# Kernel optimization log

Measured on AMD Instinct MI355X. Metric: run time of the kernel, lower is better.

Reference implementation:

```python
import jax, jax.numpy as jnp
import numpy as np

B, T, VALUE_DIM = 128, 2048, 128
ATTN_DIM, RNN_DIM, NUM_CLASSES = 10, 64, 4000
HS = (RNN_DIM + VALUE_DIM) // 2  # 96
STEPS = 32


def setup_inputs() -> dict:
    key = jax.random.key(0)
    ks = jax.random.split(key, 30)
    def p(k, shape, scale=0.08):
        return jax.random.normal(k, shape, dtype=jnp.float32) * scale
    return {
        "encoder_outputs": jax.random.normal(ks[0], (B, T, VALUE_DIM), dtype=jnp.float32),
        # 2-layer unidirectional GRU (torch layout: W_ih (3H, in), W_hh (3H, H))
        "rnn_w_ih0": p(ks[1], (3 * RNN_DIM, ATTN_DIM)),
        "rnn_w_hh0": p(ks[2], (3 * RNN_DIM, RNN_DIM)),
        "rnn_b_ih0": p(ks[3], (3 * RNN_DIM,)),
        "rnn_b_hh0": p(ks[4], (3 * RNN_DIM,)),
        "rnn_w_ih1": p(ks[5], (3 * RNN_DIM, RNN_DIM)),
        "rnn_w_hh1": p(ks[6], (3 * RNN_DIM, RNN_DIM)),
        "rnn_b_ih1": p(ks[7], (3 * RNN_DIM,)),
        "rnn_b_hh1": p(ks[8], (3 * RNN_DIM,)),
        # location-aware attention
        "attn_conv_w": p(ks[9], (ATTN_DIM, 1, 3)),   # Conv1d(1, A, k=3, pad=1)
        "attn_conv_b": p(ks[10], (ATTN_DIM,)),
        "attn_wq": p(ks[11], (ATTN_DIM, RNN_DIM)),
        "attn_bq": p(ks[12], (ATTN_DIM,)),
        "attn_wv": p(ks[13], (ATTN_DIM, VALUE_DIM)),
        "attn_bias": p(ks[14], (ATTN_DIM,)),
        "attn_score_w": p(ks[15], (ATTN_DIM,)),
        "attn_score_b": p(ks[16], (1,)),
        # classifier MLP: 192 -> 96 -> 48 -> num_classes
        "fc_w1": p(ks[17], (HS, 2 * HS)),
        "fc_b1": p(ks[18], (HS,)),
        "fc_w2": p(ks[19], (HS // 2, HS)),
        "fc_b2": p(ks[20], (HS // 2,)),
        "fc_w3": p(ks[21], (NUM_CLASSES, HS // 2)),
        "fc_b3": p(ks[22], (NUM_CLASSES,)),
        "targets_max_length": STEPS,
    }


def _gru_cell(x, h, w_ih, w_hh, b_ih, b_hh):
    gi = x @ w_ih.T + b_ih
    gh = h @ w_hh.T + b_hh
    i_r, i_z, i_n = jnp.split(gi, 3, axis=-1)
    h_r, h_z, h_n = jnp.split(gh, 3, axis=-1)
    r = jax.nn.sigmoid(i_r + h_r)
    z = jax.nn.sigmoid(i_z + h_z)
    n = jnp.tanh(i_n + r * h_n)
    return (1.0 - z) * n + z * h


def reference(encoder_outputs, rnn_w_ih0, rnn_w_hh0, rnn_b_ih0, rnn_b_hh0,
              rnn_w_ih1, rnn_w_hh1, rnn_b_ih1, rnn_b_hh1,
              attn_conv_w, attn_conv_b, attn_wq, attn_bq, attn_wv, attn_bias,
              attn_score_w, attn_score_b,
              fc_w1, fc_b1, fc_w2, fc_b2, fc_w3, fc_b3, targets_max_length):
    Bn, Tn, _ = encoder_outputs.shape
    H = rnn_w_hh0.shape[1]
    A = rnn_w_ih0.shape[1]
    # value projection is step-invariant: hoist out of the decode loop
    v_proj = jnp.einsum('btv,av->bta', encoder_outputs, attn_wv)  # (B,T,A)
    x0 = jnp.zeros((Bn, A), dtype=encoder_outputs.dtype)  # per-step RNN input

    def step(carry, _):
        h0, h1, last_attn = carry
        h0 = _gru_cell(x0, h0, rnn_w_ih0, rnn_w_hh0, rnn_b_ih0, rnn_b_hh0)
        h1 = _gru_cell(h0, h1, rnn_w_ih1, rnn_w_hh1, rnn_b_ih1, rnn_b_hh1)
        # location feature: Conv1d over previous attention weights
        loc = jax.lax.conv_general_dilated(
            last_attn[:, None, :], attn_conv_w, (1,), 'SAME',
            dimension_numbers=('NCH', 'OIH', 'NCH'))  # (B,A,T)
        loc = jnp.transpose(loc, (0, 2, 1)) + attn_conv_b  # (B,T,A)
        e = jnp.tanh((h1 @ attn_wq.T + attn_bq)[:, None, :] + v_proj + loc + attn_bias)
        score = e @ attn_score_w + attn_score_b  # (B,T)
        attn = jax.nn.softmax(score, axis=-1)
        context = jnp.einsum('bt,btv->bv', attn, encoder_outputs)  # (B,value_dim)
        hcat = jnp.concatenate([h1, context], axis=-1)  # (B, 2*HS)
        y = jax.nn.relu(hcat @ fc_w1.T + fc_b1)
        y = jax.nn.relu(y @ fc_w2.T + fc_b2)
        logits = y @ fc_w3.T + fc_b3
        logp = jax.nn.log_softmax(logits, axis=-1)
        return (h0, h1, attn), (logp, attn)

    init = (jnp.zeros((Bn, H), dtype=encoder_outputs.dtype),
            jnp.zeros((Bn, H), dtype=encoder_outputs.dtype),
            jnp.zeros((Bn, Tn), dtype=encoder_outputs.dtype))
    _, (logps, attns) = jax.lax.scan(step, init, None, length=int(targets_max_length))
    # (steps, B, ...) -> (B, steps, ...)
    return jnp.transpose(logps, (1, 0, 2)), jnp.transpose(attns, (1, 0, 2))
```

## Files before the change

kernel.cpp:

```cpp
#include <hip/hip_runtime.h>
#include <cstddef>

#define Bn 128
#define Tn 2048
#define Vn 128
#define An 10
#define Hn 64
#define NCn 4000
#define STEPSn 32
#define SCH 16
#define TCH 512
#define PREP_ROWS 32
#define PREP_T (PREP_ROWS * An)
#define NB_PREP ((Bn * Tn) / PREP_ROWS)
#define CONV_BLOCKS 512
#define LROWS 64

__device__ __forceinline__ float waveReduceSum(float v) {
    #pragma unroll
    for (int off = 32; off > 0; off >>= 1) v += __shfl_xor(v, off, 64);
    return v;
}

__device__ __forceinline__ unsigned short f2bf(float f) {
    unsigned u = __float_as_uint(f);
    u += 0x7fffu + ((u >> 16) & 1u);
    return (unsigned short)(u >> 16);
}

__device__ __forceinline__ float fexp2(float x) {
#if __has_builtin(__builtin_amdgcn_exp2f)
    return __builtin_amdgcn_exp2f(x);
#else
    return __expf(x * 0.69314718056f);
#endif
}

__global__ __launch_bounds__(640) void gru_kernel(
    const float* __restrict__ w_hh0, const float* __restrict__ b_ih0, const float* __restrict__ b_hh0,
    const float* __restrict__ w_ih1, const float* __restrict__ w_hh1,
    const float* __restrict__ b_ih1, const float* __restrict__ b_hh1,
    const float* __restrict__ wq, const float* __restrict__ bq, const float* __restrict__ abias,
    float* __restrict__ h1_all, float* __restrict__ qq_all)
{
    const int tid = threadIdx.x;
    __shared__ float h0[Hn], h1[Hn], g0[192], g1i[192], g1h[192];

    float w[64];
    float bias = 0.f;
    int role = -1, row = 0;
    const float* wsrc = nullptr;
    if (tid < 192)      { role = 0; row = tid;       wsrc = w_hh0 + row * 64; bias = b_hh0[row]; }
    else if (tid < 384) { role = 1; row = tid - 192; wsrc = w_hh1 + row * 64; bias = b_hh1[row]; }
    else if (tid < 576) { role = 2; row = tid - 384; wsrc = w_ih1 + row * 64; bias = b_ih1[row]; }
    else if (tid < 586) { role = 3; row = tid - 576; wsrc = wq    + row * 64; bias = bq[row] + abias[row]; }
    if (wsrc) {
        const float4* w4 = (const float4*)wsrc;
        #pragma unroll
        for (int k = 0; k < 16; ++k) {
            float4 v = w4[k];
            w[4*k] = v.x; w[4*k+1] = v.y; w[4*k+2] = v.z; w[4*k+3] = v.w;
        }
    }
    float bi0r = 0.f, bi0z = 0.f, bi0n = 0.f;
    if (tid < Hn) {
        bi0r = b_ih0[tid]; bi0z = b_ih0[64 + tid]; bi0n = b_ih0[128 + tid];
        h0[tid] = 0.f; h1[tid] = 0.f;
    }
    __syncthreads();

    #define DOT64(dst, src) { \
        float a0 = 0.f, a1 = 0.f, a2 = 0.f, a3 = 0.f; \
        _Pragma("unroll") \
        for (int k = 0; k < 64; k += 4) { \
            a0 = fmaf(w[k],   src[k],   a0); a1 = fmaf(w[k+1], src[k+1], a1); \
            a2 = fmaf(w[k+2], src[k+2], a2); a3 = fmaf(w[k+3], src[k+3], a3); \
        } \
        dst = bias + ((a0 + a1) + (a2 + a3)); \
    }

    for (int s = 0; s < STEPSn; ++s) {
        if (role == 0)      { DOT64(g0[row],  h0); }
        else if (role == 1) { DOT64(g1h[row], h1); }
        else if (role == 3 && s > 0) { float q; DOT64(q, h1); qq_all[(s - 1) * 16 + row] = q; }
        __syncthreads();
        if (tid < Hn) {
            float r = 1.f / (1.f + __expf(-(bi0r + g0[tid])));
            float z = 1.f / (1.f + __expf(-(bi0z + g0[64 + tid])));
            float n = tanhf(bi0n + r * g0[128 + tid]);
            h0[tid] = (1.f - z) * n + z * h0[tid];
        }
        __syncthreads();
        if (role == 2) { DOT64(g1i[row], h0); }
        __syncthreads();
        if (tid < Hn) {
            float r = 1.f / (1.f + __expf(-(g1i[tid]      + g1h[tid])));
            float z = 1.f / (1.f + __expf(-(g1i[64 + tid] + g1h[64 + tid])));
            float n = tanhf(g1i[128 + tid] + r * g1h[128 + tid]);
            float hn = (1.f - z) * n + z * h1[tid];
            h1[tid] = hn;
            h1_all[s * Hn + tid] = hn;
        }
        __syncthreads();
    }
    if (role == 3) { float q; DOT64(q, h1); qq_all[31 * 16 + row] = q; }
    #undef DOT64
}

__global__ __launch_bounds__(PREP_T) void prep_kernel(
    const float* __restrict__ enc, const float* __restrict__ wv,
    unsigned short* __restrict__ vp16)
{
    const int tid = threadIdx.x;
    __shared__ float sh[PREP_ROWS][132];
    __shared__ float wvsT[128][12];

    const size_t row0 = (size_t)blockIdx.x * PREP_ROWS;
    for (int i = tid; i < 128 * An; i += PREP_T) {
        int k = i / An, a = i - k * An;
        wvsT[k][a] = wv[a * 128 + k];
    }
    for (int i = tid; i < PREP_ROWS * 32; i += PREP_T) {
        int r = i >> 5, kq = i & 31;
        float4 v = ((const float4*)(enc + (row0 + r) * 128))[kq];
        *(float4*)&sh[r][kq * 4] = v;
    }
    __syncthreads();

    {
        int r = tid / An, a = tid - r * An;
        float acc = 0.f;
        #pragma unroll
        for (int k = 0; k < 128; k += 4) {
            float4 e = *(const float4*)&sh[r][k];
            acc = fmaf(e.x, wvsT[k][a],   acc);
            acc = fmaf(e.y, wvsT[k+1][a], acc);
            acc = fmaf(e.z, wvsT[k+2][a], acc);
            acc = fmaf(e.w, wvsT[k+3][a], acc);
        }
        vp16[(row0 + r) * An + a] = f2bf(acc);
    }
}

__global__ __launch_bounds__(1024, 4) void score_chain_kernel(
    const unsigned short* __restrict__ vp16, const float* __restrict__ qq_all,
    const float* __restrict__ conv_w, const float* __restrict__ conv_b,
    const float* __restrict__ score_w, const float* __restrict__ score_b,
    const float* __restrict__ enc, unsigned short* __restrict__ enc16,
    float* __restrict__ out_attn)
{
    const int tid = threadIdx.x;

    if (blockIdx.x >= Bn) {
        const size_t n4 = (size_t)Bn * Tn * Vn / 4;
        const float4* e4 = (const float4*)enc;
        ushort4* o4 = (ushort4*)enc16;
        for (size_t i = (size_t)(blockIdx.x - Bn) * 1024 + tid; i < n4;
             i += (size_t)CONV_BLOCKS * 1024) {
            float4 v = e4[i];
            ushort4 o;
            o.x = f2bf(v.x); o.y = f2bf(v.y); o.z = f2bf(v.z); o.w = f2bf(v.w);
            o4[i] = o;
        }
        return;
    }

    const int b = blockIdx.x;
    __shared__ float la[2][Tn + 2];
    __shared__ float red[2][16];
    __shared__ float qsh[STEPSn * 16];

    for (int i = tid; i < 2 * (Tn + 2); i += 1024) ((float*)la)[i] = 0.f;
    if (tid < STEPSn * 16) qsh[tid] = qq_all[tid];
    __syncthreads();

    const float L2E  = 1.4426950408889634f;
    const float L2E2 = 2.8853900817779268f;

    float cw0[An], cw1[An], cw2[An], qb[An], nsw2[An];
    float sb0 = score_b[0];
    #pragma unroll
    for (int a = 0; a < An; ++a) {
        cw0[a] = conv_w[3*a] * L2E2; cw1[a] = conv_w[3*a+1] * L2E2; cw2[a] = conv_w[3*a+2] * L2E2;
        qb[a] = conv_b[a] * L2E2;
        float s = score_w[a];
        sb0 += s;
        nsw2[a] = -2.f * s * L2E;
    }
    sb0 *= L2E;

    float va[2][An];
    {
        const unsigned* vpb = (const unsigned*)(vp16 + (size_t)b * Tn * An);
        #pragma unroll
        for (int half = 0; half < 2; ++half) {
            const unsigned* vpt = vpb + (size_t)(tid + half * 1024) * 5;
            #pragma unroll
            for (int k = 0; k < 5; ++k) {
                unsigned u = vpt[k];
                va[half][2*k]   = __uint_as_float(u << 16) * L2E2;
                va[half][2*k+1] = __uint_as_float(u & 0xffff0000u) * L2E2;
            }
        }
    }

    float* oa = out_attn + (size_t)b * STEPSn * Tn;
    int cur = 0;
    float inv = 1.f;

    for (int s = 0; s < STEPSn; ++s) {
        float qc[An];
        #pragma unroll
        for (int a = 0; a < An; ++a)
            qc[a] = fmaf(qsh[s * 16 + a], L2E2, qb[a]);

        const int nxt = cur ^ 1;
        float pv[2];
        float psum_loc = 0.f;
        #pragma unroll
        for (int half = 0; half < 2; ++half) {
            int t = tid + half * 1024;
            float l = la[cur][t]     * inv;
            float m = la[cur][t + 1] * inv;
            float r = la[cur][t + 2] * inv;
            float ssum = sb0;
            #pragma unroll
            for (int a = 0; a < An; ++a) {
                float arg = fmaf(cw0[a], l, fmaf(cw1[a], m, fmaf(cw2[a], r, qc[a] + va[half][a])));
                float e = fexp2(arg);
                ssum = fmaf(nsw2[a], __builtin_amdgcn_rcpf(e + 1.f), ssum);
            }
            float p = fexp2(ssum);
            la[nxt][t + 1] = p;
            pv[half] = p;
            psum_loc += p;
        }
        float wsum = waveReduceSum(psum_loc);
        if ((tid & 63) == 0) red[s & 1][tid >> 6] = wsum;
        __syncthreads();
        float tot = 0.f;
        #pragma unroll
        for (int i = 0; i < 16; ++i) tot += red[s & 1][i];
        inv = 1.f / tot;
        oa[(size_t)s * Tn + tid]        = pv[0] * inv;
        oa[(size_t)s * Tn + tid + 1024] = pv[1] * inv;
        cur = nxt;
    }
}

__global__ __launch_bounds__(256) void ctx_kernel(
    const unsigned short* __restrict__ enc16,
    const float* __restrict__ out_attn, float* __restrict__ pctx)
{
    const int bid = blockIdx.x;
    const int sc = bid & 1, tc = (bid >> 1) & 3, b = bid >> 3;
    const int t0 = tc * TCH, s0 = sc * SCH;
    const int tid = threadIdx.x;
    const int lane = tid & 63;
    const int w = __builtin_amdgcn_readfirstlane(tid >> 6);

    __shared__ float part[4 * SCH * Vn];

    float accx[SCH], accy[SCH];
    #pragma unroll
    for (int si = 0; si < SCH; ++si) { accx[si] = 0.f; accy[si] = 0.f; }

    const float* ab = out_attn + ((size_t)b * STEPSn + s0) * Tn + t0;

    for (int t4 = w * 4; t4 < TCH; t4 += 16) {
        float ex[4], ey[4];
        #pragma unroll
        for (int u = 0; u < 4; ++u) {
            unsigned uu = ((const unsigned*)enc16)[((size_t)b * Tn + t0 + t4 + u) * 64 + lane];
            ex[u] = __uint_as_float(uu << 16);
            ey[u] = __uint_as_float(uu & 0xffff0000u);
        }
        #pragma unroll
        for (int si = 0; si < SCH; ++si) {
            float4 p4 = *(const float4*)(ab + (size_t)si * Tn + t4);
            accx[si] = fmaf(p4.x, ex[0], accx[si]); accy[si] = fmaf(p4.x, ey[0], accy[si]);
            accx[si] = fmaf(p4.y, ex[1], accx[si]); accy[si] = fmaf(p4.y, ey[1], accy[si]);
            accx[si] = fmaf(p4.z, ex[2], accx[si]); accy[si] = fmaf(p4.z, ey[2], accy[si]);
            accx[si] = fmaf(p4.w, ex[3], accx[si]); accy[si] = fmaf(p4.w, ey[3], accy[si]);
        }
    }
    #pragma unroll
    for (int si = 0; si < SCH; ++si) {
        part[((w * SCH) + si) * Vn + 2 * lane]     = accx[si];
        part[((w * SCH) + si) * Vn + 2 * lane + 1] = accy[si];
    }
    __syncthreads();
    for (int o = tid; o < SCH * Vn; o += 256) {
        int si = o >> 7, v = o & (Vn - 1);
        float s2 = part[si * Vn + v] + part[(SCH + si) * Vn + v]
                 + part[(2 * SCH + si) * Vn + v] + part[(3 * SCH + si) * Vn + v];
        pctx[(((size_t)b * STEPSn + s0 + si) * 4 + tc) * Vn + v] = s2;
    }
}

__global__ __launch_bounds__(128) void mlp_kernel(
    const float* __restrict__ h1_all, const float* __restrict__ pctx,
    const float* __restrict__ fc_w1, const float* __restrict__ fc_b1,
    const float* __restrict__ fc_w2, const float* __restrict__ fc_b2,
    float* __restrict__ y2_all)
{
    const int bs = blockIdx.x;
    const int s = bs & 31;
    const int tid = threadIdx.x;
    __shared__ float hcat[192], y1[96];
    if (tid < Hn) hcat[tid] = h1_all[s * Hn + tid];
    {
        const float* pc = pctx + (size_t)bs * 4 * Vn;
        hcat[Hn + tid] = pc[tid] + pc[Vn + tid] + pc[2 * Vn + tid] + pc[3 * Vn + tid];
    }
    __syncthreads();
    if (tid < 96) {
        float acc = fc_b1[tid];
        const float4* wr = (const float4*)(fc_w1 + tid * 192);
        #pragma unroll
        for (int k = 0; k < 48; ++k) {
            float4 w = wr[k];
            acc += w.x*hcat[4*k] + w.y*hcat[4*k+1] + w.z*hcat[4*k+2] + w.w*hcat[4*k+3];
        }
        y1[tid] = fmaxf(acc, 0.f);
    }
    __syncthreads();
    if (tid < 48) {
        float acc = fc_b2[tid];
        const float4* wr = (const float4*)(fc_w2 + tid * 96);
        #pragma unroll
        for (int k = 0; k < 24; ++k) {
            float4 w = wr[k];
            acc += w.x*y1[4*k] + w.y*y1[4*k+1] + w.z*y1[4*k+2] + w.w*y1[4*k+3];
        }
        y2_all[(size_t)bs * 48 + tid] = fmaxf(acc, 0.f);
    }
}

__global__ __launch_bounds__(256) void logit_esum_kernel(
    const float* __restrict__ y2_all, const float* __restrict__ fc_w3,
    const float* __restrict__ fc_b3, float* __restrict__ esum_part)
{
    const int gx = blockIdx.x;
    const int gy = blockIdx.y;
    const int tid = threadIdx.x;
    const int lane = tid & 63;
    const int wid = __builtin_amdgcn_readfirstlane(tid >> 6);
    const int c = gx * 64 + lane;
    const bool cv = (c < NCn);

    float4 w[12];
    float bias = 0.f;
    if (cv) {
        const float4* wr = (const float4*)(fc_w3 + (size_t)c * 48);
        #pragma unroll
        for (int j = 0; j < 12; ++j) w[j] = wr[j];
        bias = fc_b3[c];
    } else {
        #pragma unroll
        for (int j = 0; j < 12; ++j) w[j] = make_float4(0.f, 0.f, 0.f, 0.f);
    }

    const int r0 = gy * LROWS + wid * 16;
    #pragma unroll
    for (int rr = 0; rr < 16; ++rr) {
        const int row = r0 + rr;
        const float* y2r = y2_all + (size_t)row * 48;
        float a0 = bias, a1 = 0.f, a2 = 0.f, a3 = 0.f;
        #pragma unroll
        for (int j = 0; j < 12; ++j) {
            float4 ww = w[j];
            a0 = fmaf(y2r[4*j],     ww.x, a0);
            a1 = fmaf(y2r[4*j + 1], ww.y, a1);
            a2 = fmaf(y2r[4*j + 2], ww.z, a2);
            a3 = fmaf(y2r[4*j + 3], ww.w, a3);
        }
        float lg = (a0 + a1) + (a2 + a3);
        float ex = cv ? __expf(lg) : 0.f;
        ex = waveReduceSum(ex);
        if (lane == 0) esum_part[(size_t)row * 64 + gx] = ex;
    }
}

__global__ __launch_bounds__(256) void logit_write_kernel(
    const float* __restrict__ y2_all, const float* __restrict__ fc_w3,
    const float* __restrict__ fc_b3, const float* __restrict__ esum_part,
    float* __restrict__ out_logp)
{
    const int gx = blockIdx.x;
    const int gy = blockIdx.y;
    const int tid = threadIdx.x;
    const int lane = tid & 63;
    const int wid = __builtin_amdgcn_readfirstlane(tid >> 6);
    const int c = gx * 64 + lane;
    const bool cv = (c < NCn);

    __shared__ float lsesh[LROWS];
    if (tid < LROWS) {
        const float* p = esum_part + (size_t)(gy * LROWS + tid) * 64;
        float s = 0.f;
        #pragma unroll
        for (int i = 0; i < 63; ++i) s += p[i];
        lsesh[tid] = logf(s);
    }

    float4 w[12];
    float bias = 0.f;
    if (cv) {
        const float4* wr = (const float4*)(fc_w3 + (size_t)c * 48);
        #pragma unroll
        for (int j = 0; j < 12; ++j) w[j] = wr[j];
        bias = fc_b3[c];
    }
    __syncthreads();

    const int r0 = gy * LROWS + wid * 16;
    if (!cv) return;
    #pragma unroll
    for (int rr = 0; rr < 16; ++rr) {
        const int row = r0 + rr;
        const float* y2r = y2_all + (size_t)row * 48;
        float a0 = bias, a1 = 0.f, a2 = 0.f, a3 = 0.f;
        #pragma unroll
        for (int j = 0; j < 12; ++j) {
            float4 ww = w[j];
            a0 = fmaf(y2r[4*j],     ww.x, a0);
            a1 = fmaf(y2r[4*j + 1], ww.y, a1);
            a2 = fmaf(y2r[4*j + 2], ww.z, a2);
            a3 = fmaf(y2r[4*j + 3], ww.w, a3);
        }
        float lg = (a0 + a1) + (a2 + a3);
        out_logp[(size_t)row * NCn + c] = lg - lsesh[wid * 16 + rr];
    }
}

extern "C" void kernel_launch(void* const* d_in, const int* in_sizes, int n_in,
                              void* d_out, int out_size, void* d_ws, size_t ws_size,
                              hipStream_t stream) {
    const float* enc    = (const float*)d_in[0];
    const float* w_hh0  = (const float*)d_in[2];
    const float* b_ih0  = (const float*)d_in[3];
    const float* b_hh0  = (const float*)d_in[4];
    const float* w_ih1  = (const float*)d_in[5];
    const float* w_hh1  = (const float*)d_in[6];
    const float* b_ih1  = (const float*)d_in[7];
    const float* b_hh1  = (const float*)d_in[8];
    const float* conv_w = (const float*)d_in[9];
    const float* conv_b = (const float*)d_in[10];
    const float* wq     = (const float*)d_in[11];
    const float* bq     = (const float*)d_in[12];
    const float* wv     = (const float*)d_in[13];
    const float* abias  = (const float*)d_in[14];
    const float* sw     = (const float*)d_in[15];
    const float* sb     = (const float*)d_in[16];
    const float* fc_w1  = (const float*)d_in[17];
    const float* fc_b1  = (const float*)d_in[18];
    const float* fc_w2  = (const float*)d_in[19];
    const float* fc_b2  = (const float*)d_in[20];
    const float* fc_w3  = (const float*)d_in[21];
    const float* fc_b3  = (const float*)d_in[22];

    size_t off = 0;
    float* wsf = (float*)d_ws;
    float* h1_all    = wsf + off; off += (size_t)STEPSn * Hn;
    float* qq_all    = wsf + off; off += (size_t)STEPSn * 16;
    float* y2_all    = wsf + off; off += (size_t)Bn * STEPSn * 48;
    float* esum_part = wsf + off; off += (size_t)Bn * STEPSn * 64;
    float* pctx      = wsf + off; off += (size_t)Bn * STEPSn * 4 * Vn;
    unsigned short* vp16  = (unsigned short*)(wsf + off); off += (size_t)Bn * Tn * An / 2;
    unsigned short* enc16 = (unsigned short*)(wsf + off); off += (size_t)Bn * Tn * Vn / 2;

    float* out_logp = (float*)d_out;
    float* out_attn = out_logp + (size_t)Bn * STEPSn * NCn;

    gru_kernel<<<1, 640, 0, stream>>>(w_hh0, b_ih0, b_hh0, w_ih1, w_hh1, b_ih1, b_hh1,
                                      wq, bq, abias, h1_all, qq_all);

    prep_kernel<<<NB_PREP, PREP_T, 0, stream>>>(enc, wv, vp16);

    score_chain_kernel<<<Bn + CONV_BLOCKS, 1024, 0, stream>>>(
        vp16, qq_all, conv_w, conv_b, sw, sb, enc, enc16, out_attn);

    ctx_kernel<<<Bn * 8, 256, 0, stream>>>(enc16, out_attn, pctx);

    mlp_kernel<<<Bn * STEPSn, 128, 0, stream>>>(h1_all, pctx, fc_w1, fc_b1, fc_w2, fc_b2, y2_all);

    logit_esum_kernel<<<dim3(63, (Bn * STEPSn) / LROWS), 256, 0, stream>>>(y2_all, fc_w3, fc_b3, esum_part);

    logit_write_kernel<<<dim3(63, (Bn * STEPSn) / LROWS), 256, 0, stream>>>(y2_all, fc_w3, fc_b3, esum_part, out_logp);
}
```

Measured before the change: 333.8 us.

## Fuse GRU recurrence into score kernel with per-step atomic flag streaming

Removes the separate single-block GRU kernel and runs the recurrence in block 0 of the score chain kernel. It publishes each step's query projection through global atomics and a step counter, which the per-batch attention blocks poll just before they need the next step. The GRU's serial latency can then overlap with the attention softmax chain instead of preceding it, and one launch is saved. This depends on block 0 being co-resident with the polling blocks, which risks deadlock if scheduling differs, and it adds spin-wait traffic on the atomics.

Measured after the change: 292.8 us. 1.14x faster.

```diff
diff --git a/kernel.cpp b/kernel.cpp
--- a/kernel.cpp
+++ b/kernel.cpp
@@ -36,84 +36,15 @@
 #endif
 }
 
-__global__ __launch_bounds__(640) void gru_kernel(
-    const float* __restrict__ w_hh0, const float* __restrict__ b_ih0, const float* __restrict__ b_hh0,
-    const float* __restrict__ w_ih1, const float* __restrict__ w_hh1,
-    const float* __restrict__ b_ih1, const float* __restrict__ b_hh1,
-    const float* __restrict__ wq, const float* __restrict__ bq, const float* __restrict__ abias,
-    float* __restrict__ h1_all, float* __restrict__ qq_all)
-{
-    const int tid = threadIdx.x;
-    __shared__ float h0[Hn], h1[Hn], g0[192], g1i[192], g1h[192];
-
-    float w[64];
-    float bias = 0.f;
-    int role = -1, row = 0;
-    const float* wsrc = nullptr;
-    if (tid < 192)      { role = 0; row = tid;       wsrc = w_hh0 + row * 64; bias = b_hh0[row]; }
-    else if (tid < 384) { role = 1; row = tid - 192; wsrc = w_hh1 + row * 64; bias = b_hh1[row]; }
-    else if (tid < 576) { role = 2; row = tid - 384; wsrc = w_ih1 + row * 64; bias = b_ih1[row]; }
-    else if (tid < 586) { role = 3; row = tid - 576; wsrc = wq    + row * 64; bias = bq[row] + abias[row]; }
-    if (wsrc) {
-        const float4* w4 = (const float4*)wsrc;
-        #pragma unroll
-        for (int k = 0; k < 16; ++k) {
-            float4 v = w4[k];
-            w[4*k] = v.x; w[4*k+1] = v.y; w[4*k+2] = v.z; w[4*k+3] = v.w;
-        }
-    }
-    float bi0r = 0.f, bi0z = 0.f, bi0n = 0.f;
-    if (tid < Hn) {
-        bi0r = b_ih0[tid]; bi0z = b_ih0[64 + tid]; bi0n = b_ih0[128 + tid];
-        h0[tid] = 0.f; h1[tid] = 0.f;
-    }
-    __syncthreads();
-
-    #define DOT64(dst, src) { \
-        float a0 = 0.f, a1 = 0.f, a2 = 0.f, a3 = 0.f; \
-        _Pragma("unroll") \
-        for (int k = 0; k < 64; k += 4) { \
-            a0 = fmaf(w[k],   src[k],   a0); a1 = fmaf(w[k+1], src[k+1], a1); \
-            a2 = fmaf(w[k+2], src[k+2], a2); a3 = fmaf(w[k+3], src[k+3], a3); \
-        } \
-        dst = bias + ((a0 + a1) + (a2 + a3)); \
-    }
-
-    for (int s = 0; s < STEPSn; ++s) {
-        if (role == 0)      { DOT64(g0[row],  h0); }
-        else if (role == 1) { DOT64(g1h[row], h1); }
-        else if (role == 3 && s > 0) { float q; DOT64(q, h1); qq_all[(s - 1) * 16 + row] = q; }
-        __syncthreads();
-        if (tid < Hn) {
-            float r = 1.f / (1.f + __expf(-(bi0r + g0[tid])));
-            float z = 1.f / (1.f + __expf(-(bi0z + g0[64 + tid])));
-            float n = tanhf(bi0n + r * g0[128 + tid]);
-            h0[tid] = (1.f - z) * n + z * h0[tid];
-        }
-        __syncthreads();
-        if (role == 2) { DOT64(g1i[row], h0); }
-        __syncthreads();
-        if (tid < Hn) {
-            float r = 1.f / (1.f + __expf(-(g1i[tid]      + g1h[tid])));
-            float z = 1.f / (1.f + __expf(-(g1i[64 + tid] + g1h[64 + tid])));
-            float n = tanhf(g1i[128 + tid] + r * g1h[128 + tid]);
-            float hn = (1.f - z) * n + z * h1[tid];
-            h1[tid] = hn;
-            h1_all[s * Hn + tid] = hn;
-        }
-        __syncthreads();
-    }
-    if (role == 3) { float q; DOT64(q, h1); qq_all[31 * 16 + row] = q; }
-    #undef DOT64
-}
-
 __global__ __launch_bounds__(PREP_T) void prep_kernel(
     const float* __restrict__ enc, const float* __restrict__ wv,
-    unsigned short* __restrict__ vp16)
+    unsigned short* __restrict__ vp16, unsigned* __restrict__ qsync)
 {
     const int tid = threadIdx.x;
     __shared__ float sh[PREP_ROWS][132];
     __shared__ float wvsT[128][12];
+
+    if (blockIdx.x == 0 && tid == 0) qsync[0] = 0u;
 
     const size_t row0 = (size_t)blockIdx.x * PREP_ROWS;
     for (int i = tid; i < 128 * An; i += PREP_T) {
@@ -143,19 +74,97 @@
 }
 
 __global__ __launch_bounds__(1024, 4) void score_chain_kernel(
-    const unsigned short* __restrict__ vp16, const float* __restrict__ qq_all,
+    const unsigned short* __restrict__ vp16,
+    const float* __restrict__ w_hh0, const float* __restrict__ b_ih0, const float* __restrict__ b_hh0,
+    const float* __restrict__ w_ih1, const float* __restrict__ w_hh1,
+    const float* __restrict__ b_ih1, const float* __restrict__ b_hh1,
+    const float* __restrict__ wq, const float* __restrict__ bq, const float* __restrict__ abias,
     const float* __restrict__ conv_w, const float* __restrict__ conv_b,
     const float* __restrict__ score_w, const float* __restrict__ score_b,
     const float* __restrict__ enc, unsigned short* __restrict__ enc16,
+    float* __restrict__ h1_all, unsigned* __restrict__ qsync,
     float* __restrict__ out_attn)
 {
     const int tid = threadIdx.x;
 
-    if (blockIdx.x >= Bn) {
+    if (blockIdx.x == 0) {
+        __shared__ float h0[Hn], h1[Hn], g0[192], g1i[192], g1h[192];
+        float w[64];
+        float bias = 0.f;
+        int role = -1, row = 0;
+        const float* wsrc = nullptr;
+        if (tid < 192)      { role = 0; row = tid;       wsrc = w_hh0 + row * 64; bias = b_hh0[row]; }
+        else if (tid < 384) { role = 1; row = tid - 192; wsrc = w_hh1 + row * 64; bias = b_hh1[row]; }
+        else if (tid < 576) { role = 2; row = tid - 384; wsrc = w_ih1 + row * 64; bias = b_ih1[row]; }
+        else if (tid < 576 + An) { role = 3; row = tid - 576; wsrc = wq + row * 64; bias = bq[row] + abias[row]; }
+        if (wsrc) {
+            const float4* w4 = (const float4*)wsrc;
+            #pragma unroll
+            for (int k = 0; k < 16; ++k) {
+                float4 v = w4[k];
+                w[4*k] = v.x; w[4*k+1] = v.y; w[4*k+2] = v.z; w[4*k+3] = v.w;
+            }
+        }
+        float bi0r = 0.f, bi0z = 0.f, bi0n = 0.f;
+        if (tid < Hn) {
+            bi0r = b_ih0[tid]; bi0z = b_ih0[64 + tid]; bi0n = b_ih0[128 + tid];
+            h0[tid] = 0.f; h1[tid] = 0.f;
+        }
+        __syncthreads();
+
+        #define DOT64(dst, src) { \
+            float a0 = 0.f, a1 = 0.f, a2 = 0.f, a3 = 0.f; \
+            _Pragma("unroll") \
+            for (int k = 0; k < 64; k += 4) { \
+                a0 = fmaf(w[k],   src[k],   a0); a1 = fmaf(w[k+1], src[k+1], a1); \
+                a2 = fmaf(w[k+2], src[k+2], a2); a3 = fmaf(w[k+3], src[k+3], a3); \
+            } \
+            dst = bias + ((a0 + a1) + (a2 + a3)); \
+        }
+
+        for (int s = 0; s < STEPSn; ++s) {
+            if (role == 0)      { DOT64(g0[row],  h0); }
+            else if (role == 1) { DOT64(g1h[row], h1); }
+            else if (role == 3 && s > 0) {
+                float q; DOT64(q, h1);
+                atomicExch(&qsync[1 + (s - 1) * 16 + row], __float_as_uint(q));
+            }
+            __syncthreads();
+            if (tid == 0 && s > 0) atomicAdd(&qsync[0], 1u);
+            if (tid < Hn) {
+                float r = 1.f / (1.f + __expf(-(bi0r + g0[tid])));
+                float z = 1.f / (1.f + __expf(-(bi0z + g0[64 + tid])));
+                float n = tanhf(bi0n + r * g0[128 + tid]);
+                h0[tid] = (1.f - z) * n + z * h0[tid];
+            }
+            __syncthreads();
+            if (role == 2) { DOT64(g1i[row], h0); }
+            __syncthreads();
+            if (tid < Hn) {
+                float r = 1.f / (1.f + __expf(-(g1i[tid]      + g1h[tid])));
+                float z = 1.f / (1.f + __expf(-(g1i[64 + tid] + g1h[64 + tid])));
+                float n = tanhf(g1i[128 + tid] + r * g1h[128 + tid]);
+                float hn = (1.f - z) * n + z * h1[tid];
+                h1[tid] = hn;
+                h1_all[s * Hn + tid] = hn;
+            }
+            __syncthreads();
+        }
+        if (role == 3) {
+            float q; DOT64(q, h1);
+            atomicExch(&qsync[1 + 31 * 16 + row], __float_as_uint(q));
+        }
+        __syncthreads();
+        if (tid == 0) atomicAdd(&qsync[0], 1u);
+        #undef DOT64
+        return;
+    }
+
+    if (blockIdx.x > Bn) {
         const size_t n4 = (size_t)Bn * Tn * Vn / 4;
         const float4* e4 = (const float4*)enc;
         ushort4* o4 = (ushort4*)enc16;
-        for (size_t i = (size_t)(blockIdx.x - Bn) * 1024 + tid; i < n4;
+        for (size_t i = (size_t)(blockIdx.x - Bn - 1) * 1024 + tid; i < n4;
              i += (size_t)CONV_BLOCKS * 1024) {
             float4 v = e4[i];
             ushort4 o;
@@ -165,13 +174,16 @@
         return;
     }
 
-    const int b = blockIdx.x;
+    const int b = blockIdx.x - 1;
     __shared__ float la[2][Tn + 2];
     __shared__ float red[2][16];
-    __shared__ float qsh[STEPSn * 16];
+    __shared__ float qsh2[2][16];
 
     for (int i = tid; i < 2 * (Tn + 2); i += 1024) ((float*)la)[i] = 0.f;
-    if (tid < STEPSn * 16) qsh[tid] = qq_all[tid];
+    if (tid < 64) {
+        if (tid == 0) { while (atomicAdd(qsync, 0u) < 1u) ; }
+        if (tid < An) qsh2[0][tid] = __uint_as_float(atomicAdd(&qsync[1 + tid], 0u));
+    }
     __syncthreads();
 
     const float L2E  = 1.4426950408889634f;
@@ -212,7 +224,15 @@
         float qc[An];
         #pragma unroll
         for (int a = 0; a < An; ++a)
-            qc[a] = fmaf(qsh[s * 16 + a], L2E2, qb[a]);
+            qc[a] = fmaf(qsh2[s & 1][a], L2E2, qb[a]);
+
+        if (s + 1 < STEPSn && (tid >> 6) == ((s + 1) & 15)) {
+            const int lane = tid & 63;
+            if (lane == 0) { while (atomicAdd(qsync, 0u) < (unsigned)(s + 2)) ; }
+            if (lane < An)
+                qsh2[(s + 1) & 1][lane] =
+                    __uint_as_float(atomicAdd(&qsync[1 + (s + 1) * 16 + lane], 0u));
+        }
 
         const int nxt = cur ^ 1;
         float pv[2];
@@ -463,7 +483,7 @@
     size_t off = 0;
     float* wsf = (float*)d_ws;
     float* h1_all    = wsf + off; off += (size_t)STEPSn * Hn;
-    float* qq_all    = wsf + off; off += (size_t)STEPSn * 16;
+    unsigned* qsync  = (unsigned*)(wsf + off); off += 1 + STEPSn * 16;
     float* y2_all    = wsf + off; off += (size_t)Bn * STEPSn * 48;
     float* esum_part = wsf + off; off += (size_t)Bn * STEPSn * 64;
     float* pctx      = wsf + off; off += (size_t)Bn * STEPSn * 4 * Vn;
@@ -473,13 +493,12 @@
     float* out_logp = (float*)d_out;
     float* out_attn = out_logp + (size_t)Bn * STEPSn * NCn;
 
-    gru_kernel<<<1, 640, 0, stream>>>(w_hh0, b_ih0, b_hh0, w_ih1, w_hh1, b_ih1, b_hh1,
-                                      wq, bq, abias, h1_all, qq_all);
-
-    prep_kernel<<<NB_PREP, PREP_T, 0, stream>>>(enc, wv, vp16);
-
-    score_chain_kernel<<<Bn + CONV_BLOCKS, 1024, 0, stream>>>(
-        vp16, qq_all, conv_w, conv_b, sw, sb, enc, enc16, out_attn);
+    prep_kernel<<<NB_PREP, PREP_T, 0, stream>>>(enc, wv, vp16, qsync);
+
+    score_chain_kernel<<<1 + Bn + CONV_BLOCKS, 1024, 0, stream>>>(
+        vp16, w_hh0, b_ih0, b_hh0, w_ih1, w_hh1, b_ih1, b_hh1,
+        wq, bq, abias, conv_w, conv_b, sw, sb, enc, enc16,
+        h1_all, qsync, out_attn);
 
     ctx_kernel<<<Bn * 8, 256, 0, stream>>>(enc16, out_attn, pctx);
 
```
